# Kernel optimization log

Hardware: AMD Instinct MI355X
Metric: run time of the kernel (lower is better)

The kernel has to match this reference:

```python
import jax, jax.numpy as jnp
import numpy as np
from jax import lax

B, S, HID = 2, 2048, 1024
HK, HV, DK, DV = 16, 16, 64, 64
KCONV = 4
NORM_EPS = 1e-5
KEY_DIM = HK * DK
VAL_DIM = HV * DV
CCH = 2 * KEY_DIM + VAL_DIM  # qkv channels


def setup_inputs() -> dict:
    key = jax.random.key(0)
    ks = jax.random.split(key, 8)
    std = 0.02
    hidden_states = jax.random.normal(ks[0], (B, S, HID), jnp.float32)
    w_qkv = jax.random.normal(ks[1], (CCH, HID), jnp.float32) * std
    w_ab = jax.random.normal(ks[2], (2 * HV + VAL_DIM, HID), jnp.float32) * std
    w_conv = jax.random.normal(ks[3], (CCH, KCONV), jnp.float32) * std  # depthwise kernel
    A_log = jnp.log(jax.random.uniform(ks[4], (HV,), jnp.float32, 1e-3, 16.0))
    dt = jnp.exp(jax.random.uniform(ks[5], (HV,), jnp.float32) * (np.log(0.1) - np.log(0.001)) + np.log(0.001))
    dt = jnp.maximum(dt, 1e-4)
    dt_bias = dt + jnp.log(-jnp.expm1(-dt))
    rms_w = jnp.ones((DV,), jnp.float32)
    w_o = jax.random.normal(ks[6], (HID, VAL_DIM), jnp.float32) * (std / np.sqrt(2 * 24))
    return dict(hidden_states=hidden_states, w_qkv=w_qkv, w_ab=w_ab, w_conv=w_conv,
                A_log=A_log, dt_bias=dt_bias, rms_w=rms_w, w_o=w_o)


def _l2norm(x, eps=1e-6):
    return x * lax.rsqrt(jnp.sum(x * x, axis=-1, keepdims=True) + eps)


def reference(hidden_states, w_qkv, w_ab, w_conv, A_log, dt_bias, rms_w, w_o):
    qkv = hidden_states @ w_qkv.T                       # [B,S,CCH]
    ab = hidden_states @ w_ab.T                         # [B,S,2H+VAL_DIM]
    a = ab[..., :HV]
    b = ab[..., HV:2 * HV]
    gate = ab[..., 2 * HV:]
    # causal depthwise conv1d (kernel KCONV, left pad KCONV-1) + silu
    xp = jnp.pad(qkv, ((0, 0), (KCONV - 1, 0), (0, 0)))
    conv = sum(xp[:, i:i + S, :] * w_conv[:, i] for i in range(KCONV))
    qkv = jax.nn.silu(conv)
    q = qkv[..., :KEY_DIM].reshape(B, S, HK, DK)
    k = qkv[..., KEY_DIM:2 * KEY_DIM].reshape(B, S, HK, DK)
    v = qkv[..., 2 * KEY_DIM:].reshape(B, S, HV, DV)
    # HV == HK -> no repeat_interleave needed
    beta = jax.nn.sigmoid(b)                            # [B,S,H]
    g = -jnp.exp(A_log) * jax.nn.softplus(a + dt_bias)  # [B,S,H]
    q = _l2norm(q)
    k = _l2norm(k)
    scale = DK ** -0.5

    def step(h, x):
        qt, kt, vt, gt, bt = x                          # [B,H,D*] / [B,H]
        h = h * jnp.exp(gt)[..., None, None]            # decay: [B,H,DK,DV]
        kv = jnp.einsum('bhk,bhkv->bhv', kt, h)
        delta = bt[..., None] * (vt - kv)               # delta-rule error
        h = h + jnp.einsum('bhk,bhv->bhkv', kt, delta)  # rank-1 update
        ot = jnp.einsum('bhk,bhkv->bhv', qt * scale, h)
        return h, ot

    xs = (jnp.moveaxis(q, 1, 0), jnp.moveaxis(k, 1, 0), jnp.moveaxis(v, 1, 0),
          jnp.moveaxis(g, 1, 0), jnp.moveaxis(beta, 1, 0))
    h0 = jnp.zeros((B, HV, DK, DV), jnp.float32)
    _, o = lax.scan(step, h0, xs)                       # [S,B,H,DV]
    o = jnp.moveaxis(o, 0, 1)                           # [B,S,H,DV]
    o = o * jax.nn.silu(gate.reshape(B, S, HV, DV))
    o = o * lax.rsqrt(jnp.mean(o * o, axis=-1, keepdims=True) + NORM_EPS) * rms_w
    o = o.reshape(B, S, VAL_DIM) @ w_o.T                # [B,S,HID]
    return o
```

## Files before the change

### kernel.cpp

```cpp
#include <hip/hip_runtime.h>
#include <stdint.h>
#include <math.h>

#define NPAD 4224

typedef float  f32x4_t __attribute__((ext_vector_type(4)));
typedef __bf16 bfx8_t  __attribute__((ext_vector_type(8)));
typedef __bf16 bfx4_t  __attribute__((ext_vector_type(4)));

#define F4(p)  (*reinterpret_cast<const float4*>(p))
#define F4W(p) (*reinterpret_cast<float4*>(p))

__device__ __forceinline__ void gload_lds16(const void* g, void* l) {
  __builtin_amdgcn_global_load_lds((const __attribute__((address_space(1))) void*)g,
                                   (__attribute__((address_space(3))) void*)l, 16, 0, 0);
}

__device__ __forceinline__ float sigmoidf_fast(float x) { return 1.f / (1.f + __expf(-x)); }
__device__ __forceinline__ float siluf(float x) { return x * sigmoidf_fast(x); }

__device__ __forceinline__ float allreduce64(float v) {
#pragma unroll
  for (int m = 1; m < 64; m <<= 1) v += __shfl_xor(v, m, 64);
  return v;
}

__device__ __forceinline__ bfx4_t to_bf4(float4 v) {
  bfx4_t o; o[0] = (__bf16)v.x; o[1] = (__bf16)v.y; o[2] = (__bf16)v.z; o[3] = (__bf16)v.w;
  return o;
}

__device__ __forceinline__ uint32_t bf2pack(float a, float b) {
  union { __bf16 h[2]; uint32_t u; } x;
  x.h[0] = (__bf16)a; x.h[1] = (__bf16)b; return x.u;
}

__global__ __launch_bounds__(256) void cvt_f32_bf16(const float* __restrict__ in,
                                                    __bf16* __restrict__ out) {
  int i = blockIdx.x * 256 + threadIdx.x;
  float4 v = reinterpret_cast<const float4*>(in)[i];
  reinterpret_cast<bfx4_t*>(out)[i] = to_bf4(v);
}

__global__ __launch_bounds__(256) void cvt_weights(const float* __restrict__ wqkv,
                                                   const float* __restrict__ wab,
                                                   __bf16* __restrict__ Wb) {
  int i = blockIdx.x * 256 + threadIdx.x;
  int e = i * 4;
  int row = e >> 10, col = e & 1023;
  float4 v;
  if (row < 3072)      v = *reinterpret_cast<const float4*>(wqkv + e);
  else if (row < 4128) v = *reinterpret_cast<const float4*>(wab + ((row - 3072) << 10) + col);
  else                 v = make_float4(0.f, 0.f, 0.f, 0.f);
  reinterpret_cast<bfx4_t*>(Wb)[i] = to_bf4(v);
}

__global__ __launch_bounds__(256, 2) void gemm_bt(const __bf16* __restrict__ A,
                                                  const __bf16* __restrict__ Bm,
                                                  float* __restrict__ C,
                                                  int K, int lda, int ldb, int ldc) {
  __shared__ __align__(16) __bf16 As[128 * 64];
  __shared__ __align__(16) __bf16 Bs[128 * 64];
  const int tid = threadIdx.x;
  const int w = tid >> 6, lane = tid & 63;
  const int tm = blockIdx.x & 31, tn = blockIdx.x >> 5;
  const int wr = w >> 1, wc = w & 1;
  const int srow = lane >> 3, scol = (lane & 7) * 8;

  f32x4_t acc[4][4];
#pragma unroll
  for (int i = 0; i < 4; i++)
#pragma unroll
    for (int j = 0; j < 4; j++) acc[i][j] = f32x4_t{0.f, 0.f, 0.f, 0.f};

  const __bf16* Abase = A + (size_t)(tm * 128 + srow) * lda + scol;
  const __bf16* Bbase = Bm + (size_t)(tn * 128 + srow) * ldb + scol;

  for (int kk = 0; kk < K; kk += 64) {
#pragma unroll
    for (int r = 0; r < 4; r++) {
      const int rr = (r * 4 + w) * 8;
      gload_lds16(Abase + (size_t)rr * lda + kk, &As[rr * 64]);
      gload_lds16(Bbase + (size_t)rr * ldb + kk, &Bs[rr * 64]);
    }
    __syncthreads();
#pragma unroll
    for (int ks = 0; ks < 2; ks++) {
      bfx8_t af[4], bfr[4];
#pragma unroll
      for (int i = 0; i < 4; i++) {
        af[i]  = *reinterpret_cast<const bfx8_t*>(&As[(wr * 64 + i * 16 + (lane & 15)) * 64 + ks * 32 + (lane >> 4) * 8]);
        bfr[i] = *reinterpret_cast<const bfx8_t*>(&Bs[(wc * 64 + i * 16 + (lane & 15)) * 64 + ks * 32 + (lane >> 4) * 8]);
      }
#pragma unroll
      for (int i = 0; i < 4; i++)
#pragma unroll
        for (int j = 0; j < 4; j++)
          acc[i][j] = __builtin_amdgcn_mfma_f32_16x16x32_bf16(af[i], bfr[j], acc[i][j], 0, 0, 0);
    }
    __syncthreads();
  }
  const int crow = tm * 128 + wr * 64 + (lane >> 4) * 4;
  const int ccol = tn * 128 + wc * 64 + (lane & 15);
#pragma unroll
  for (int i = 0; i < 4; i++)
#pragma unroll
    for (int j = 0; j < 4; j++)
#pragma unroll
      for (int r = 0; r < 4; r++)
        C[(size_t)(crow + i * 16 + r) * ldc + ccol + j * 16] = acc[i][j][r];
}

__global__ __launch_bounds__(256, 2) void gemm_bt_b16(const __bf16* __restrict__ A,
                                                      const __bf16* __restrict__ Bm,
                                                      __bf16* __restrict__ C,
                                                      int K, int lda, int ldb, int ldc) {
  __shared__ __align__(16) __bf16 As[128 * 64];
  __shared__ __align__(16) __bf16 Bs[128 * 64];
  const int tid = threadIdx.x;
  const int w = tid >> 6, lane = tid & 63;
  const int tm = blockIdx.x & 31, tn = blockIdx.x >> 5;
  const int wr = w >> 1, wc = w & 1;
  const int srow = lane >> 3, scol = (lane & 7) * 8;

  f32x4_t acc[4][4];
#pragma unroll
  for (int i = 0; i < 4; i++)
#pragma unroll
    for (int j = 0; j < 4; j++) acc[i][j] = f32x4_t{0.f, 0.f, 0.f, 0.f};

  const __bf16* Abase = A + (size_t)(tm * 128 + srow) * lda + scol;
  const __bf16* Bbase = Bm + (size_t)(tn * 128 + srow) * ldb + scol;

  for (int kk = 0; kk < K; kk += 64) {
#pragma unroll
    for (int r = 0; r < 4; r++) {
      const int rr = (r * 4 + w) * 8;
      gload_lds16(Abase + (size_t)rr * lda + kk, &As[rr * 64]);
      gload_lds16(Bbase + (size_t)rr * ldb + kk, &Bs[rr * 64]);
    }
    __syncthreads();
#pragma unroll
    for (int ks = 0; ks < 2; ks++) {
      bfx8_t af[4], bfr[4];
#pragma unroll
      for (int i = 0; i < 4; i++) {
        af[i]  = *reinterpret_cast<const bfx8_t*>(&As[(wr * 64 + i * 16 + (lane & 15)) * 64 + ks * 32 + (lane >> 4) * 8]);
        bfr[i] = *reinterpret_cast<const bfx8_t*>(&Bs[(wc * 64 + i * 16 + (lane & 15)) * 64 + ks * 32 + (lane >> 4) * 8]);
      }
#pragma unroll
      for (int i = 0; i < 4; i++)
#pragma unroll
        for (int j = 0; j < 4; j++)
          acc[i][j] = __builtin_amdgcn_mfma_f32_16x16x32_bf16(af[i], bfr[j], acc[i][j], 0, 0, 0);
    }
    __syncthreads();
  }
  const int crow = tm * 128 + wr * 64 + (lane >> 4) * 4;
  const int ccol = tn * 128 + wc * 64 + (lane & 15);
#pragma unroll
  for (int i = 0; i < 4; i++)
#pragma unroll
    for (int j = 0; j < 4; j++)
#pragma unroll
      for (int r = 0; r < 4; r++)
        C[(size_t)(crow + i * 16 + r) * ldc + ccol + j * 16] = (__bf16)acc[i][j][r];
}

__global__ __launch_bounds__(256) void prep_kernel(
    const __bf16* __restrict__ Y, const float* __restrict__ w_conv,
    const float* __restrict__ A_log, const float* __restrict__ dt_bias,
    float* __restrict__ qs, float* __restrict__ ks_, float* __restrict__ vs,
    float* __restrict__ gbuf, float* __restrict__ bbuf) {
  const int blk = blockIdx.x;
  const int b = blk >> 11, s = blk & 2047;
  const int tid = threadIdx.x;
  const int w = tid >> 6, lane = tid & 63;

  float x[12];
#pragma unroll
  for (int j = 0; j < 12; j++) {
    const int c = tid + 256 * j;
    const float4 wc = *reinterpret_cast<const float4*>(w_conv + c * 4);
    const float* wcp = reinterpret_cast<const float*>(&wc);
    float acc = 0.f;
#pragma unroll
    for (int i = 0; i < 4; i++) {
      const int r = s - 3 + i;
      const float v = (r >= 0) ? (float)Y[(size_t)(b * 2048 + r) * NPAD + c] : 0.f;
      acc = fmaf(v, wcp[i], acc);
    }
    x[j] = siluf(acc);
  }

#pragma unroll
  for (int j = 0; j < 4; j++) {
    const float sq = allreduce64(x[j] * x[j]);
    const float sk = allreduce64(x[j + 4] * x[j + 4]);
    const float rq = rsqrtf(sq + 1e-6f) * 0.125f;
    const float rk = rsqrtf(sk + 1e-6f);
    const int head = 4 * j + w;
    const size_t base = ((size_t)(b * 16 + head) * 2048 + s) * 64 + lane;
    qs[base] = x[j] * rq;
    ks_[base] = x[j + 4] * rk;
    vs[base] = x[8 + j];
  }

  const __bf16* yab = Y + (size_t)blk * NPAD + 3072;
  if (tid < 16) {
    float a = (float)yab[tid] + dt_bias[tid];
    float sp = (a > 20.f) ? a : log1pf(expf(a));
    gbuf[(size_t)(b * 16 + tid) * 2048 + s] = -expf(A_log[tid]) * sp;
  } else if (tid < 32) {
    int t = tid - 16;
    bbuf[(size_t)(b * 16 + t) * 2048 + s] = 1.f / (1.f + expf(-(float)yab[16 + t]));
  }
}


__global__ __launch_bounds__(256, 3) void chunkA(
    const float* __restrict__ ks_, const float* __restrict__ vs,
    const float* __restrict__ gbuf, const float* __restrict__ bbuf,
    float* __restrict__ Dvg, __bf16* __restrict__ Wgb,
    float* __restrict__ Mg, float* __restrict__ PTg, float* __restrict__ egb) {
  const int task = blockIdx.x, bh = task >> 5, cc = task & 31;
  const int tid = threadIdx.x;
  const int w = tid >> 6, lane = tid & 63;
  __shared__ __align__(16) char regA[18432];
  __shared__ __align__(16) float Ks[64 * 68];
  __shared__ __align__(16) char regC[9216];
  __shared__ float xbc[2][128];
  __shared__ float gcs[64], bcs[64];
  float* At   = (float*)regA;
  __bf16* XTb = (__bf16*)regA;
  __bf16* Kb   = (__bf16*)regC;
  __bf16* KdTb = (__bf16*)regC;

  const size_t cb = ((size_t)bh * 2048 + cc * 64) * 64;
  { int s = tid >> 2, d0 = (tid & 3) * 16;
#pragma unroll
    for (int i = 0; i < 4; i++) {
      float4 v = F4(&ks_[cb + (size_t)s * 64 + d0 + 4 * i]);
      F4W(&Ks[s * 68 + d0 + 4 * i]) = v;
      *reinterpret_cast<bfx4_t*>(&Kb[s * 72 + d0 + 4 * i]) = to_bf4(v);
    }
  }
  if (tid < 64) {
    float gv = gbuf[(size_t)bh * 2048 + cc * 64 + tid];
    bcs[tid] = bbuf[(size_t)bh * 2048 + cc * 64 + tid];
#pragma unroll
    for (int off = 1; off < 64; off <<= 1) {
      float n = __shfl_up(gv, (unsigned)off, 64);
      if (tid >= off) gv += n;
    }
    gcs[tid] = gv;
  }
  __syncthreads();

  const int hh = tid >> 7, cI = tid & 127;
  float vpre[32];
  if (cI < 64) {
#pragma unroll
    for (int r = 0; r < 32; r++)
      vpre[r] = vs[cb + (size_t)(hh * 32 + r) * 64 + cI];
  }

  {
    bfx8_t aS[2];
#pragma unroll
    for (int kh = 0; kh < 2; kh++)
      aS[kh] = *reinterpret_cast<const bfx8_t*>(&Kb[(16 * w + (lane & 15)) * 72 + kh * 32 + (lane >> 4) * 8]);
#pragma unroll
    for (int j = 0; j < 4; j++) {
      if (j < w) {
#pragma unroll
        for (int r = 0; r < 4; r++)
          At[(16 * w + (lane >> 4) * 4 + r) * 68 + 16 * j + (lane & 15)] = 0.f;
      } else {
        f32x4_t acc = {0.f, 0.f, 0.f, 0.f};
#pragma unroll
        for (int kh = 0; kh < 2; kh++) {
          bfx8_t bS = *reinterpret_cast<const bfx8_t*>(&Kb[(16 * j + (lane & 15)) * 72 + kh * 32 + (lane >> 4) * 8]);
          acc = __builtin_amdgcn_mfma_f32_16x16x32_bf16(aS[kh], bS, acc, 0, 0, 0);
        }
        const int t = 16 * j + (lane & 15);
        const float bt = bcs[t], gt = gcs[t];
#pragma unroll
        for (int r = 0; r < 4; r++) {
          const int s = 16 * w + (lane >> 4) * 4 + r;
          At[s * 68 + t] = (t > s) ? bt * __expf(gt - gcs[s]) * acc[r] : 0.f;
        }
      }
    }
  }
  __syncthreads();

  float X[32];
  if (cI < 64) {
#pragma unroll
    for (int r = 0; r < 32; r++) X[r] = bcs[hh * 32 + r] * vpre[r];
  } else {
#pragma unroll
    for (int r = 0; r < 32; r++) {
      int s = hh * 32 + r;
      X[r] = bcs[s] * __expf(gcs[s]) * Ks[s * 68 + (cI - 64)];
    }
  }

#pragma unroll
  for (int s = 0; s < 64; ++s) {
    if (hh == (s >> 5)) xbc[s & 1][cI] = X[s & 31];
    __syncthreads();
    float xs = xbc[s & 1][cI];
    const float* atrow = &At[s * 68 + hh * 32];
#pragma unroll
    for (int j = 0; j < 8; j++) {
      float4 a4 = F4(atrow + 4 * j);
      X[4 * j + 0] = fmaf(-a4.x, xs, X[4 * j + 0]);
      X[4 * j + 1] = fmaf(-a4.y, xs, X[4 * j + 1]);
      X[4 * j + 2] = fmaf(-a4.z, xs, X[4 * j + 2]);
      X[4 * j + 3] = fmaf(-a4.w, xs, X[4 * j + 3]);
    }
  }
  __syncthreads();

  if (cI < 64) {
#pragma unroll
    for (int r = 0; r < 32; r++)
      Dvg[(size_t)task * 4096 + (size_t)(hh * 32 + r) * 64 + cI] = X[r];
  } else {
#pragma unroll
    for (int r = 0; r < 32; r++)
      Wgb[(size_t)task * 4096 + (size_t)(hh * 32 + r) * 64 + (cI - 64)] = (__bf16)X[r];
  }
#pragma unroll
  for (int i = 0; i < 16; i++)
    *reinterpret_cast<uint32_t*>(&XTb[cI * 72 + hh * 32 + 2 * i]) = bf2pack(X[2 * i], X[2 * i + 1]);
  {
    int s = tid >> 2, d0 = (tid & 3) * 16;
    float ek = __expf(gcs[63] - gcs[s]);
#pragma unroll
    for (int i = 0; i < 4; i++) {
      float4 v = F4(&Ks[s * 68 + d0 + 4 * i]);
      KdTb[(d0 + 4 * i + 0) * 72 + s] = (__bf16)(v.x * ek);
      KdTb[(d0 + 4 * i + 1) * 72 + s] = (__bf16)(v.y * ek);
      KdTb[(d0 + 4 * i + 2) * 72 + s] = (__bf16)(v.z * ek);
      KdTb[(d0 + 4 * i + 3) * 72 + s] = (__bf16)(v.w * ek);
    }
  }
  __syncthreads();

  {
    bfx8_t aM[2], aP[2];
#pragma unroll
    for (int kh = 0; kh < 2; kh++) {
      aM[kh] = *reinterpret_cast<const bfx8_t*>(&KdTb[(16 * w + (lane & 15)) * 72 + kh * 32 + (lane >> 4) * 8]);
      aP[kh] = *reinterpret_cast<const bfx8_t*>(&XTb [(16 * w + (lane & 15)) * 72 + kh * 32 + (lane >> 4) * 8]);
    }
#pragma unroll
    for (int j = 0; j < 4; j++) {
      f32x4_t mAcc = {0.f, 0.f, 0.f, 0.f}, pAcc = {0.f, 0.f, 0.f, 0.f};
#pragma unroll
      for (int kh = 0; kh < 2; kh++) {
        bfx8_t bW = *reinterpret_cast<const bfx8_t*>(&XTb [(64 + 16 * j + (lane & 15)) * 72 + kh * 32 + (lane >> 4) * 8]);
        bfx8_t bK = *reinterpret_cast<const bfx8_t*>(&KdTb[(16 * j + (lane & 15)) * 72 + kh * 32 + (lane >> 4) * 8]);
        mAcc = __builtin_amdgcn_mfma_f32_16x16x32_bf16(aM[kh], bW, mAcc, 0, 0, 0);
        pAcc = __builtin_amdgcn_mfma_f32_16x16x32_bf16(aP[kh], bK, pAcc, 0, 0, 0);
      }
#pragma unroll
      for (int r = 0; r < 4; r++) {
        const int drow = 16 * w + (lane >> 4) * 4 + r;
        const int ecol = 16 * j + (lane & 15);
        const int ge = ecol >> 2;
        const int ges = (ge & 8) | ((ge & 7) ^ (drow & 7));
        Mg [(size_t)task * 4096 + drow * 64 + ges * 4 + (ecol & 3)] = mAcc[r];
        PTg[(size_t)task * 4096 + drow * 64 + ecol] = pAcc[r];
      }
    }
  }
  if (tid == 0) egb[task] = __expf(gcs[63]);
}

__global__ __launch_bounds__(64) void chunkB(
    const float* __restrict__ Mg, const float* __restrict__ PTg,
    const float* __restrict__ egb, float* __restrict__ hTg) {
  const int bh = blockIdx.x & 31, vq = blockIdx.x >> 5;
  const int tid = threadIdx.x;
  const int tv = tid >> 4, td = tid & 15;
  __shared__ __align__(16) float Ml[2][64 * 64];
  __shared__ __align__(16) float hT[8 * 68];

  float h[2][4];
#pragma unroll
  for (int r = 0; r < 2; r++)
#pragma unroll
    for (int c = 0; c < 4; c++) h[r][c] = 0.f;
#pragma unroll
  for (int r = 0; r < 2; r++)
#pragma unroll
    for (int c = 0; c < 4; c++) hT[(tv * 2 + r) * 68 + c * 16 + td] = 0.f;

  const char* mb = (const char*)(Mg + (size_t)bh * 32 * 4096);
#pragma unroll
  for (int j = 0; j < 16; j++)
    gload_lds16(mb + j * 1024 + tid * 16, &Ml[0][j * 256]);

  const int kk = (td & 7) << 2;
  int cur = 0;
  for (int cch = 0; cch < 32; ++cch) {
    const size_t tb = ((size_t)bh * 32 + cch) * 4096;
    asm volatile("s_waitcnt vmcnt(0)" ::: "memory");
    __builtin_amdgcn_sched_barrier(0);
    if (cch < 31) {
#pragma unroll
      for (int j = 0; j < 16; j++)
        gload_lds16(mb + (size_t)(cch + 1) * 16384 + j * 1024 + tid * 16,
                    &Ml[cur ^ 1][j * 256]);
    }
    float ptc[2][4];
#pragma unroll
    for (int r = 0; r < 2; r++)
#pragma unroll
      for (int c = 0; c < 4; c++)
        ptc[r][c] = PTg[tb + (size_t)(vq * 8 + tv * 2 + r) * 64 + c * 16 + td];
    const float egc = egb[bh * 32 + cch];
#pragma unroll
    for (int r = 0; r < 2; r++)
#pragma unroll
      for (int c = 0; c < 4; c++)
        hTg[tb + (size_t)(vq * 8 + tv * 2 + r) * 64 + c * 16 + td] = h[r][c];
    float acc[2][4] = {};
#pragma unroll
    for (int e0 = 0; e0 < 64; e0 += 4) {
      const int es = (e0 & 32) | ((e0 & 28) ^ kk);
      float4 h4[2], m4[4];
#pragma unroll
      for (int r = 0; r < 2; r++) h4[r] = F4(&hT[(tv * 2 + r) * 68 + e0]);
#pragma unroll
      for (int c = 0; c < 4; c++) m4[c] = F4(&Ml[cur][(c * 16 + td) * 64 + es]);
#pragma unroll
      for (int r = 0; r < 2; r++)
#pragma unroll
        for (int c = 0; c < 4; c++) {
          acc[r][c] = fmaf(h4[r].x, m4[c].x, acc[r][c]);
          acc[r][c] = fmaf(h4[r].y, m4[c].y, acc[r][c]);
          acc[r][c] = fmaf(h4[r].z, m4[c].z, acc[r][c]);
          acc[r][c] = fmaf(h4[r].w, m4[c].w, acc[r][c]);
        }
    }
#pragma unroll
    for (int r = 0; r < 2; r++)
#pragma unroll
      for (int c = 0; c < 4; c++)
        h[r][c] = egc * h[r][c] - acc[r][c] + ptc[r][c];
#pragma unroll
    for (int r = 0; r < 2; r++)
#pragma unroll
      for (int c = 0; c < 4; c++) hT[(tv * 2 + r) * 68 + c * 16 + td] = h[r][c];
    cur ^= 1;
  }
}

__global__ __launch_bounds__(256, 3) void chunkC(
    const float* __restrict__ qs, const float* __restrict__ ks_,
    const float* __restrict__ gbuf, const float* __restrict__ Dvg,
    const __bf16* __restrict__ Wgb, const float* __restrict__ hTg,
    float* __restrict__ o_raw) {
  const int task = blockIdx.x, bh = task >> 5, cc = task & 31;
  const int b = bh >> 4, hd = bh & 15;
  const int tid = threadIdx.x;
  const int w = tid >> 6, lane = tid & 63;
  __shared__ __align__(16) __bf16 cQb[64 * 72];
  __shared__ __align__(16) char  regK[9216];
  __shared__ __align__(16) __bf16 cWb[64 * 72];
  __shared__ __align__(16) __bf16 hTb[64 * 72];
  __shared__ __align__(16) __bf16 Smb[64 * 72];
  __shared__ float gcs[64];
  __bf16* cKb = (__bf16*)regK;
  __bf16* dTb = (__bf16*)regK;

  const size_t cb = ((size_t)bh * 2048 + cc * 64) * 64;
  { int s = tid >> 2, d0 = (tid & 3) * 16;
#pragma unroll
    for (int i = 0; i < 4; i++) {
      *reinterpret_cast<bfx4_t*>(&cQb[s * 72 + d0 + 4 * i]) = to_bf4(F4(&qs [cb + (size_t)s * 64 + d0 + 4 * i]));
      *reinterpret_cast<bfx4_t*>(&cKb[s * 72 + d0 + 4 * i]) = to_bf4(F4(&ks_[cb + (size_t)s * 64 + d0 + 4 * i]));
      *reinterpret_cast<bfx4_t*>(&hTb[s * 72 + d0 + 4 * i]) = to_bf4(F4(&hTg[(size_t)task * 4096 + (size_t)s * 64 + d0 + 4 * i]));
    }
    const bfx8_t* wp = reinterpret_cast<const bfx8_t*>(&Wgb[(size_t)task * 4096 + (size_t)s * 64 + d0]);
    *reinterpret_cast<bfx8_t*>(&cWb[s * 72 + d0]) = wp[0];
    *reinterpret_cast<bfx8_t*>(&cWb[s * 72 + d0 + 8]) = wp[1];
  }
  if (tid < 64) {
    float gv = gbuf[(size_t)bh * 2048 + cc * 64 + tid];
#pragma unroll
    for (int off = 1; off < 64; off <<= 1) {
      float n = __shfl_up(gv, (unsigned)off, 64);
      if (tid >= off) gv += n;
    }
    gcs[tid] = gv;
  }
  __syncthreads();

  f32x4_t qh[4];
  {
    bfx8_t aQ[2];
#pragma unroll
    for (int kh = 0; kh < 2; kh++)
      aQ[kh] = *reinterpret_cast<const bfx8_t*>(&cQb[(16 * w + (lane & 15)) * 72 + kh * 32 + (lane >> 4) * 8]);
#pragma unroll
    for (int j = 0; j < 4; j++) {
      f32x4_t sAcc = {0.f, 0.f, 0.f, 0.f};
      qh[j] = f32x4_t{0.f, 0.f, 0.f, 0.f};
#pragma unroll
      for (int kh = 0; kh < 2; kh++) {
        bfx8_t bK = *reinterpret_cast<const bfx8_t*>(&cKb[(16 * j + (lane & 15)) * 72 + kh * 32 + (lane >> 4) * 8]);
        bfx8_t bH = *reinterpret_cast<const bfx8_t*>(&hTb[(16 * j + (lane & 15)) * 72 + kh * 32 + (lane >> 4) * 8]);
        sAcc = __builtin_amdgcn_mfma_f32_16x16x32_bf16(aQ[kh], bK, sAcc, 0, 0, 0);
        qh[j] = __builtin_amdgcn_mfma_f32_16x16x32_bf16(aQ[kh], bH, qh[j], 0, 0, 0);
      }
      const int s = 16 * j + (lane & 15);
      const float gs = gcs[s];
#pragma unroll
      for (int r = 0; r < 4; r++) {
        const int t = 16 * w + (lane >> 4) * 4 + r;
        float sv = (s <= t) ? __expf(gcs[t] - gs) * sAcc[r] : 0.f;
        Smb[t * 72 + s] = (__bf16)sv;
      }
    }
  }
  __syncthreads();

  {
    bfx8_t aW[2];
#pragma unroll
    for (int kh = 0; kh < 2; kh++)
      aW[kh] = *reinterpret_cast<const bfx8_t*>(&cWb[(16 * w + (lane & 15)) * 72 + kh * 32 + (lane >> 4) * 8]);
#pragma unroll
    for (int j = 0; j < 4; j++) {
      f32x4_t u = {0.f, 0.f, 0.f, 0.f};
#pragma unroll
      for (int kh = 0; kh < 2; kh++) {
        bfx8_t bH = *reinterpret_cast<const bfx8_t*>(&hTb[(16 * j + (lane & 15)) * 72 + kh * 32 + (lane >> 4) * 8]);
        u = __builtin_amdgcn_mfma_f32_16x16x32_bf16(aW[kh], bH, u, 0, 0, 0);
      }
      const int v = 16 * j + (lane & 15);
#pragma unroll
      for (int r = 0; r < 4; r++) {
        const int s = 16 * w + (lane >> 4) * 4 + r;
        float dl = Dvg[(size_t)task * 4096 + (size_t)s * 64 + v] - u[r];
        dTb[v * 72 + s] = (__bf16)dl;
      }
    }
  }
  __syncthreads();

  {
    bfx8_t aS2[2];
#pragma unroll
    for (int kh = 0; kh < 2; kh++)
      aS2[kh] = *reinterpret_cast<const bfx8_t*>(&Smb[(16 * w + (lane & 15)) * 72 + kh * 32 + (lane >> 4) * 8]);
    float esc[4];
#pragma unroll
    for (int r = 0; r < 4; r++) esc[r] = __expf(gcs[16 * w + (lane >> 4) * 4 + r]);
#pragma unroll
    for (int j = 0; j < 4; j++) {
#pragma unroll
      for (int r = 0; r < 4; r++) qh[j][r] *= esc[r];
#pragma unroll
      for (int kh = 0; kh < 2; kh++) {
        bfx8_t bD = *reinterpret_cast<const bfx8_t*>(&dTb[(16 * j + (lane & 15)) * 72 + kh * 32 + (lane >> 4) * 8]);
        qh[j] = __builtin_amdgcn_mfma_f32_16x16x32_bf16(aS2[kh], bD, qh[j], 0, 0, 0);
      }
      const int v = 16 * j + (lane & 15);
#pragma unroll
      for (int r = 0; r < 4; r++) {
        const int t = 16 * w + (lane >> 4) * 4 + r;
        o_raw[(((size_t)b * 2048 + cc * 64 + t) * 16 + hd) * 64 + v] = qh[j][r];
      }
    }
  }
}

__global__ __launch_bounds__(256) void gate_rms(
    const float* __restrict__ o_raw, const __bf16* __restrict__ Y,
    const float* __restrict__ rms_w, __bf16* __restrict__ o2b) {
  const int blk = blockIdx.x;
  const int tid = threadIdx.x;
  const int H = tid >> 4, d0 = (tid & 15) * 4;
  const size_t ob = (size_t)blk * 1024 + H * 64 + d0;
  float4 o = *reinterpret_cast<const float4*>(o_raw + ob);
  bfx4_t gb = *reinterpret_cast<const bfx4_t*>(Y + (size_t)blk * NPAD + 3104 + H * 64 + d0);
  float o2[4];
  o2[0] = o.x * siluf((float)gb[0]); o2[1] = o.y * siluf((float)gb[1]);
  o2[2] = o.z * siluf((float)gb[2]); o2[3] = o.w * siluf((float)gb[3]);
  float ssq = o2[0] * o2[0] + o2[1] * o2[1] + o2[2] * o2[2] + o2[3] * o2[3];
  ssq += __shfl_xor(ssq, 1, 64);
  ssq += __shfl_xor(ssq, 2, 64);
  ssq += __shfl_xor(ssq, 4, 64);
  ssq += __shfl_xor(ssq, 8, 64);
  const float scale = rsqrtf(ssq * (1.f / 64.f) + 1e-5f);
  bfx4_t r;
#pragma unroll
  for (int i = 0; i < 4; i++) r[i] = (__bf16)(o2[i] * scale * rms_w[d0 + i]);
  *reinterpret_cast<bfx4_t*>(o2b + ob) = r;
}

extern "C" void kernel_launch(void* const* d_in, const int* in_sizes, int n_in,
                              void* d_out, int out_size, void* d_ws, size_t ws_size,
                              hipStream_t stream) {
  (void)in_sizes; (void)n_in; (void)out_size; (void)ws_size;
  const float* hidden = (const float*)d_in[0];
  const float* w_qkv  = (const float*)d_in[1];
  const float* w_ab   = (const float*)d_in[2];
  const float* w_conv = (const float*)d_in[3];
  const float* A_log  = (const float*)d_in[4];
  const float* dt_b   = (const float*)d_in[5];
  const float* rms_w  = (const float*)d_in[6];
  const float* w_o    = (const float*)d_in[7];
  float* out = (float*)d_out;

  char* ws = (char*)d_ws;
  size_t off = 0;
  auto alloc = [&](size_t bytes) { void* p = ws + off; off += (bytes + 255) & ~(size_t)255; return p; };
  __bf16* Xb   = (__bf16*)alloc((size_t)4096 * 1024 * 2);
  __bf16* Wb   = (__bf16*)alloc((size_t)NPAD * 1024 * 2);
  __bf16* Wob  = (__bf16*)alloc((size_t)1024 * 1024 * 2);
  __bf16* Y    = (__bf16*)alloc((size_t)4096 * NPAD * 2);
  float* qs    = (float*)alloc((size_t)32 * 2048 * 64 * 4);
  float* ks    = (float*)alloc((size_t)32 * 2048 * 64 * 4);
  float* vs    = (float*)alloc((size_t)32 * 2048 * 64 * 4);
  float* gbuf  = (float*)alloc((size_t)32 * 2048 * 4);
  float* bbuf  = (float*)alloc((size_t)32 * 2048 * 4);
  float* Dvg   = (float*)alloc((size_t)1024 * 4096 * 4);
  __bf16* Wgb  = (__bf16*)alloc((size_t)1024 * 4096 * 2);
  float* Mg    = (float*)alloc((size_t)1024 * 4096 * 4);
  float* PTg   = (float*)alloc((size_t)1024 * 4096 * 4);
  float* hTg   = (float*)alloc((size_t)1024 * 4096 * 4);
  float* egb   = (float*)alloc((size_t)1024 * 4);
  __bf16* o2b  = (__bf16*)alloc((size_t)4096 * 1024 * 2);
  float* o_raw = (float*)Xb;

  cvt_f32_bf16<<<4096, 256, 0, stream>>>(hidden, Xb);
  cvt_weights<<<4224, 256, 0, stream>>>(w_qkv, w_ab, Wb);
  cvt_f32_bf16<<<1024, 256, 0, stream>>>(w_o, Wob);
  gemm_bt_b16<<<32 * 33, 256, 0, stream>>>(Xb, Wb, Y, 1024, 1024, 1024, NPAD);
  prep_kernel<<<4096, 256, 0, stream>>>(Y, w_conv, A_log, dt_b, qs, ks, vs, gbuf, bbuf);
  chunkA<<<1024, 256, 0, stream>>>(ks, vs, gbuf, bbuf, Dvg, Wgb, Mg, PTg, egb);
  chunkB<<<256, 64, 0, stream>>>(Mg, PTg, egb, hTg);
  chunkC<<<1024, 256, 0, stream>>>(qs, ks, gbuf, Dvg, Wgb, hTg, o_raw);
  gate_rms<<<4096, 256, 0, stream>>>(o_raw, Y, rms_w, o2b);
  gemm_bt<<<32 * 8, 256, 0, stream>>>(o2b, Wob, out, 1024, 1024, 1024, 1024);
}
```

Baseline: 359.8 us.

## Store q/k/v intermediates in bf16 and vectorize prep kernel

The prep kernel now writes q, k and v as bf16 instead of fp32. Each thread handles 8 contiguous channels with 16-byte loads and does the per-head L2 norm through 8-lane shuffles rather than full 64-lane allreduces. chunkA and chunkC read bf16 directly, which removes the fp32 K shared-memory copy and one barrier, and chunkA's occupancy hint rises from 3 to 4 blocks. This halves the bytes written and read for q/k/v but rounds v and k to bf16 earlier, slightly changing numerics in the fp32 paths that previously used fp32 k/v.

```diff
diff --git a/kernel.cpp b/kernel.cpp
--- a/kernel.cpp
+++ b/kernel.cpp
@@ -10,6 +10,8 @@
 
 #define F4(p)  (*reinterpret_cast<const float4*>(p))
 #define F4W(p) (*reinterpret_cast<float4*>(p))
+#define BF8(p)  (*reinterpret_cast<const bfx8_t*>(p))
+#define BF8W(p) (*reinterpret_cast<bfx8_t*>(p))
 
 __device__ __forceinline__ void gload_lds16(const void* g, void* l) {
   __builtin_amdgcn_global_load_lds((const __attribute__((address_space(1))) void*)g,
@@ -18,12 +20,6 @@
 
 __device__ __forceinline__ float sigmoidf_fast(float x) { return 1.f / (1.f + __expf(-x)); }
 __device__ __forceinline__ float siluf(float x) { return x * sigmoidf_fast(x); }
-
-__device__ __forceinline__ float allreduce64(float v) {
-#pragma unroll
-  for (int m = 1; m < 64; m <<= 1) v += __shfl_xor(v, m, 64);
-  return v;
-}
 
 __device__ __forceinline__ bfx4_t to_bf4(float4 v) {
   bfx4_t o; o[0] = (__bf16)v.x; o[1] = (__bf16)v.y; o[2] = (__bf16)v.z; o[3] = (__bf16)v.w;
@@ -89,8 +85,8 @@
       bfx8_t af[4], bfr[4];
 #pragma unroll
       for (int i = 0; i < 4; i++) {
-        af[i]  = *reinterpret_cast<const bfx8_t*>(&As[(wr * 64 + i * 16 + (lane & 15)) * 64 + ks * 32 + (lane >> 4) * 8]);
-        bfr[i] = *reinterpret_cast<const bfx8_t*>(&Bs[(wc * 64 + i * 16 + (lane & 15)) * 64 + ks * 32 + (lane >> 4) * 8]);
+        af[i]  = BF8(&As[(wr * 64 + i * 16 + (lane & 15)) * 64 + ks * 32 + (lane >> 4) * 8]);
+        bfr[i] = BF8(&Bs[(wc * 64 + i * 16 + (lane & 15)) * 64 + ks * 32 + (lane >> 4) * 8]);
       }
 #pragma unroll
       for (int i = 0; i < 4; i++)
@@ -145,8 +141,8 @@
       bfx8_t af[4], bfr[4];
 #pragma unroll
       for (int i = 0; i < 4; i++) {
-        af[i]  = *reinterpret_cast<const bfx8_t*>(&As[(wr * 64 + i * 16 + (lane & 15)) * 64 + ks * 32 + (lane >> 4) * 8]);
-        bfr[i] = *reinterpret_cast<const bfx8_t*>(&Bs[(wc * 64 + i * 16 + (lane & 15)) * 64 + ks * 32 + (lane >> 4) * 8]);
+        af[i]  = BF8(&As[(wr * 64 + i * 16 + (lane & 15)) * 64 + ks * 32 + (lane >> 4) * 8]);
+        bfr[i] = BF8(&Bs[(wc * 64 + i * 16 + (lane & 15)) * 64 + ks * 32 + (lane >> 4) * 8]);
       }
 #pragma unroll
       for (int i = 0; i < 4; i++)
@@ -167,43 +163,56 @@
         C[(size_t)(crow + i * 16 + r) * ldc + ccol + j * 16] = (__bf16)acc[i][j][r];
 }
 
-__global__ __launch_bounds__(256) void prep_kernel(
+__global__ __launch_bounds__(384) void prep_kernel(
     const __bf16* __restrict__ Y, const float* __restrict__ w_conv,
     const float* __restrict__ A_log, const float* __restrict__ dt_bias,
-    float* __restrict__ qs, float* __restrict__ ks_, float* __restrict__ vs,
+    __bf16* __restrict__ qs, __bf16* __restrict__ ks_, __bf16* __restrict__ vs,
     float* __restrict__ gbuf, float* __restrict__ bbuf) {
   const int blk = blockIdx.x;
   const int b = blk >> 11, s = blk & 2047;
   const int tid = threadIdx.x;
-  const int w = tid >> 6, lane = tid & 63;
-
-  float x[12];
-#pragma unroll
-  for (int j = 0; j < 12; j++) {
-    const int c = tid + 256 * j;
-    const float4 wc = *reinterpret_cast<const float4*>(w_conv + c * 4);
-    const float* wcp = reinterpret_cast<const float*>(&wc);
-    float acc = 0.f;
-#pragma unroll
-    for (int i = 0; i < 4; i++) {
-      const int r = s - 3 + i;
-      const float v = (r >= 0) ? (float)Y[(size_t)(b * 2048 + r) * NPAD + c] : 0.f;
-      acc = fmaf(v, wcp[i], acc);
-    }
-    x[j] = siluf(acc);
-  }
-
-#pragma unroll
-  for (int j = 0; j < 4; j++) {
-    const float sq = allreduce64(x[j] * x[j]);
-    const float sk = allreduce64(x[j + 4] * x[j + 4]);
-    const float rq = rsqrtf(sq + 1e-6f) * 0.125f;
-    const float rk = rsqrtf(sk + 1e-6f);
-    const int head = 4 * j + w;
-    const size_t base = ((size_t)(b * 16 + head) * 2048 + s) * 64 + lane;
-    qs[base] = x[j] * rq;
-    ks_[base] = x[j + 4] * rk;
-    vs[base] = x[8 + j];
+  const int c0 = tid * 8;
+
+  bfx8_t yv[4], z8;
+#pragma unroll
+  for (int q = 0; q < 8; q++) z8[q] = (__bf16)0.f;
+#pragma unroll
+  for (int i = 0; i < 4; i++) {
+    const int r = s - 3 + i;
+    yv[i] = (r >= 0) ? BF8(&Y[(size_t)(b * 2048 + r) * NPAD + c0]) : z8;
+  }
+  float x[8];
+#pragma unroll
+  for (int q = 0; q < 8; q++) {
+    const float4 wq = F4(&w_conv[(c0 + q) * 4]);
+    float acc = fmaf((float)yv[0][q], wq.x,
+                fmaf((float)yv[1][q], wq.y,
+                fmaf((float)yv[2][q], wq.z, (float)yv[3][q] * wq.w)));
+    x[q] = siluf(acc);
+  }
+
+  const int sec = tid >> 7;
+  const int head = (tid >> 3) & 15;
+  const int d0 = (tid & 7) * 8;
+  const size_t base = ((size_t)(b * 16 + head) * 2048 + s) * 64 + d0;
+  bfx8_t outv;
+  if (sec < 2) {
+    float ss = 0.f;
+#pragma unroll
+    for (int q = 0; q < 8; q++) ss = fmaf(x[q], x[q], ss);
+    ss += __shfl_xor(ss, 1, 64);
+    ss += __shfl_xor(ss, 2, 64);
+    ss += __shfl_xor(ss, 4, 64);
+    float rs = rsqrtf(ss + 1e-6f);
+    if (sec == 0) rs *= 0.125f;
+#pragma unroll
+    for (int q = 0; q < 8; q++) outv[q] = (__bf16)(x[q] * rs);
+    if (sec == 0) BF8W(&qs[base]) = outv;
+    else          BF8W(&ks_[base]) = outv;
+  } else {
+#pragma unroll
+    for (int q = 0; q < 8; q++) outv[q] = (__bf16)x[q];
+    BF8W(&vs[base]) = outv;
   }
 
   const __bf16* yab = Y + (size_t)blk * NPAD + 3072;
@@ -218,8 +227,8 @@
 }
 
 
-__global__ __launch_bounds__(256, 3) void chunkA(
-    const float* __restrict__ ks_, const float* __restrict__ vs,
+__global__ __launch_bounds__(256, 4) void chunkA(
+    const __bf16* __restrict__ ks_, const __bf16* __restrict__ vs,
     const float* __restrict__ gbuf, const float* __restrict__ bbuf,
     float* __restrict__ Dvg, __bf16* __restrict__ Wgb,
     float* __restrict__ Mg, float* __restrict__ PTg, float* __restrict__ egb) {
@@ -227,7 +236,6 @@
   const int tid = threadIdx.x;
   const int w = tid >> 6, lane = tid & 63;
   __shared__ __align__(16) char regA[18432];
-  __shared__ __align__(16) float Ks[64 * 68];
   __shared__ __align__(16) char regC[9216];
   __shared__ float xbc[2][128];
   __shared__ float gcs[64], bcs[64];
@@ -237,14 +245,11 @@
   __bf16* KdTb = (__bf16*)regC;
 
   const size_t cb = ((size_t)bh * 2048 + cc * 64) * 64;
-  { int s = tid >> 2, d0 = (tid & 3) * 16;
-#pragma unroll
-    for (int i = 0; i < 4; i++) {
-      float4 v = F4(&ks_[cb + (size_t)s * 64 + d0 + 4 * i]);
-      F4W(&Ks[s * 68 + d0 + 4 * i]) = v;
-      *reinterpret_cast<bfx4_t*>(&Kb[s * 72 + d0 + 4 * i]) = to_bf4(v);
-    }
-  }
+  const int sr = tid >> 2, sd0 = (tid & 3) * 16;
+  bfx8_t kst0 = BF8(&ks_[cb + (size_t)sr * 64 + sd0]);
+  bfx8_t kst1 = BF8(&ks_[cb + (size_t)sr * 64 + sd0 + 8]);
+  BF8W(&Kb[sr * 72 + sd0]) = kst0;
+  BF8W(&Kb[sr * 72 + sd0 + 8]) = kst1;
   if (tid < 64) {
     float gv = gbuf[(size_t)bh * 2048 + cc * 64 + tid];
     bcs[tid] = bbuf[(size_t)bh * 2048 + cc * 64 + tid];
@@ -262,14 +267,14 @@
   if (cI < 64) {
 #pragma unroll
     for (int r = 0; r < 32; r++)
-      vpre[r] = vs[cb + (size_t)(hh * 32 + r) * 64 + cI];
+      vpre[r] = (float)vs[cb + (size_t)(hh * 32 + r) * 64 + cI];
   }
 
   {
     bfx8_t aS[2];
 #pragma unroll
     for (int kh = 0; kh < 2; kh++)
-      aS[kh] = *reinterpret_cast<const bfx8_t*>(&Kb[(16 * w + (lane & 15)) * 72 + kh * 32 + (lane >> 4) * 8]);
+      aS[kh] = BF8(&Kb[(16 * w + (lane & 15)) * 72 + kh * 32 + (lane >> 4) * 8]);
 #pragma unroll
     for (int j = 0; j < 4; j++) {
       if (j < w) {
@@ -280,7 +285,7 @@
         f32x4_t acc = {0.f, 0.f, 0.f, 0.f};
 #pragma unroll
         for (int kh = 0; kh < 2; kh++) {
-          bfx8_t bS = *reinterpret_cast<const bfx8_t*>(&Kb[(16 * j + (lane & 15)) * 72 + kh * 32 + (lane >> 4) * 8]);
+          bfx8_t bS = BF8(&Kb[(16 * j + (lane & 15)) * 72 + kh * 32 + (lane >> 4) * 8]);
           acc = __builtin_amdgcn_mfma_f32_16x16x32_bf16(aS[kh], bS, acc, 0, 0, 0);
         }
         const int t = 16 * j + (lane & 15);
@@ -293,7 +298,6 @@
       }
     }
   }
-  __syncthreads();
 
   float X[32];
   if (cI < 64) {
@@ -303,7 +307,7 @@
 #pragma unroll
     for (int r = 0; r < 32; r++) {
       int s = hh * 32 + r;
-      X[r] = bcs[s] * __expf(gcs[s]) * Ks[s * 68 + (cI - 64)];
+      X[r] = bcs[s] * __expf(gcs[s]) * (float)Kb[s * 72 + (cI - 64)];
     }
   }
 
@@ -337,15 +341,11 @@
   for (int i = 0; i < 16; i++)
     *reinterpret_cast<uint32_t*>(&XTb[cI * 72 + hh * 32 + 2 * i]) = bf2pack(X[2 * i], X[2 * i + 1]);
   {
-    int s = tid >> 2, d0 = (tid & 3) * 16;
-    float ek = __expf(gcs[63] - gcs[s]);
-#pragma unroll
-    for (int i = 0; i < 4; i++) {
-      float4 v = F4(&Ks[s * 68 + d0 + 4 * i]);
-      KdTb[(d0 + 4 * i + 0) * 72 + s] = (__bf16)(v.x * ek);
-      KdTb[(d0 + 4 * i + 1) * 72 + s] = (__bf16)(v.y * ek);
-      KdTb[(d0 + 4 * i + 2) * 72 + s] = (__bf16)(v.z * ek);
-      KdTb[(d0 + 4 * i + 3) * 72 + s] = (__bf16)(v.w * ek);
+    const float ek = __expf(gcs[63] - gcs[sr]);
+#pragma unroll
+    for (int i = 0; i < 8; i++) {
+      KdTb[(sd0 + i) * 72 + sr]     = (__bf16)((float)kst0[i] * ek);
+      KdTb[(sd0 + 8 + i) * 72 + sr] = (__bf16)((float)kst1[i] * ek);
     }
   }
   __syncthreads();
@@ -354,16 +354,16 @@
     bfx8_t aM[2], aP[2];
 #pragma unroll
     for (int kh = 0; kh < 2; kh++) {
-      aM[kh] = *reinterpret_cast<const bfx8_t*>(&KdTb[(16 * w + (lane & 15)) * 72 + kh * 32 + (lane >> 4) * 8]);
-      aP[kh] = *reinterpret_cast<const bfx8_t*>(&XTb [(16 * w + (lane & 15)) * 72 + kh * 32 + (lane >> 4) * 8]);
+      aM[kh] = BF8(&KdTb[(16 * w + (lane & 15)) * 72 + kh * 32 + (lane >> 4) * 8]);
+      aP[kh] = BF8(&XTb [(16 * w + (lane & 15)) * 72 + kh * 32 + (lane >> 4) * 8]);
     }
 #pragma unroll
     for (int j = 0; j < 4; j++) {
       f32x4_t mAcc = {0.f, 0.f, 0.f, 0.f}, pAcc = {0.f, 0.f, 0.f, 0.f};
 #pragma unroll
       for (int kh = 0; kh < 2; kh++) {
-        bfx8_t bW = *reinterpret_cast<const bfx8_t*>(&XTb [(64 + 16 * j + (lane & 15)) * 72 + kh * 32 + (lane >> 4) * 8]);
-        bfx8_t bK = *reinterpret_cast<const bfx8_t*>(&KdTb[(16 * j + (lane & 15)) * 72 + kh * 32 + (lane >> 4) * 8]);
+        bfx8_t bW = BF8(&XTb [(64 + 16 * j + (lane & 15)) * 72 + kh * 32 + (lane >> 4) * 8]);
+        bfx8_t bK = BF8(&KdTb[(16 * j + (lane & 15)) * 72 + kh * 32 + (lane >> 4) * 8]);
         mAcc = __builtin_amdgcn_mfma_f32_16x16x32_bf16(aM[kh], bW, mAcc, 0, 0, 0);
         pAcc = __builtin_amdgcn_mfma_f32_16x16x32_bf16(aP[kh], bK, pAcc, 0, 0, 0);
       }
@@ -462,7 +462,7 @@
 }
 
 __global__ __launch_bounds__(256, 3) void chunkC(
-    const float* __restrict__ qs, const float* __restrict__ ks_,
+    const __bf16* __restrict__ qs, const __bf16* __restrict__ ks_,
     const float* __restrict__ gbuf, const float* __restrict__ Dvg,
     const __bf16* __restrict__ Wgb, const float* __restrict__ hTg,
     float* __restrict__ o_raw) {
@@ -481,15 +481,16 @@
 
   const size_t cb = ((size_t)bh * 2048 + cc * 64) * 64;
   { int s = tid >> 2, d0 = (tid & 3) * 16;
-#pragma unroll
-    for (int i = 0; i < 4; i++) {
-      *reinterpret_cast<bfx4_t*>(&cQb[s * 72 + d0 + 4 * i]) = to_bf4(F4(&qs [cb + (size_t)s * 64 + d0 + 4 * i]));
-      *reinterpret_cast<bfx4_t*>(&cKb[s * 72 + d0 + 4 * i]) = to_bf4(F4(&ks_[cb + (size_t)s * 64 + d0 + 4 * i]));
-      *reinterpret_cast<bfx4_t*>(&hTb[s * 72 + d0 + 4 * i]) = to_bf4(F4(&hTg[(size_t)task * 4096 + (size_t)s * 64 + d0 + 4 * i]));
-    }
-    const bfx8_t* wp = reinterpret_cast<const bfx8_t*>(&Wgb[(size_t)task * 4096 + (size_t)s * 64 + d0]);
-    *reinterpret_cast<bfx8_t*>(&cWb[s * 72 + d0]) = wp[0];
-    *reinterpret_cast<bfx8_t*>(&cWb[s * 72 + d0 + 8]) = wp[1];
+    BF8W(&cQb[s * 72 + d0])     = BF8(&qs [cb + (size_t)s * 64 + d0]);
+    BF8W(&cQb[s * 72 + d0 + 8]) = BF8(&qs [cb + (size_t)s * 64 + d0 + 8]);
+    BF8W(&cKb[s * 72 + d0])     = BF8(&ks_[cb + (size_t)s * 64 + d0]);
+    BF8W(&cKb[s * 72 + d0 + 8]) = BF8(&ks_[cb + (size_t)s * 64 + d0 + 8]);
+#pragma unroll
+    for (int i = 0; i < 4; i++)
+      *reinterpret_cast<bfx4_t*>(&hTb[s * 72 + d0 + 4 * i]) =
+          to_bf4(F4(&hTg[(size_t)task * 4096 + (size_t)s * 64 + d0 + 4 * i]));
+    BF8W(&cWb[s * 72 + d0])     = BF8(&Wgb[(size_t)task * 4096 + (size_t)s * 64 + d0]);
+    BF8W(&cWb[s * 72 + d0 + 8]) = BF8(&Wgb[(size_t)task * 4096 + (size_t)s * 64 + d0 + 8]);
   }
   if (tid < 64) {
     float gv = gbuf[(size_t)bh * 2048 + cc * 64 + tid];
@@ -507,15 +508,15 @@
     bfx8_t aQ[2];
 #pragma unroll
     for (int kh = 0; kh < 2; kh++)
-      aQ[kh] = *reinterpret_cast<const bfx8_t*>(&cQb[(16 * w + (lane & 15)) * 72 + kh * 32 + (lane >> 4) * 8]);
+      aQ[kh] = BF8(&cQb[(16 * w + (lane & 15)) * 72 + kh * 32 + (lane >> 4) * 8]);
 #pragma unroll
     for (int j = 0; j < 4; j++) {
       f32x4_t sAcc = {0.f, 0.f, 0.f, 0.f};
       qh[j] = f32x4_t{0.f, 0.f, 0.f, 0.f};
 #pragma unroll
       for (int kh = 0; kh < 2; kh++) {
-        bfx8_t bK = *reinterpret_cast<const bfx8_t*>(&cKb[(16 * j + (lane & 15)) * 72 + kh * 32 + (lane >> 4) * 8]);
-        bfx8_t bH = *reinterpret_cast<const bfx8_t*>(&hTb[(16 * j + (lane & 15)) * 72 + kh * 32 + (lane >> 4) * 8]);
+        bfx8_t bK = BF8(&cKb[(16 * j + (lane & 15)) * 72 + kh * 32 + (lane >> 4) * 8]);
+        bfx8_t bH = BF8(&hTb[(16 * j + (lane & 15)) * 72 + kh * 32 + (lane >> 4) * 8]);
         sAcc = __builtin_amdgcn_mfma_f32_16x16x32_bf16(aQ[kh], bK, sAcc, 0, 0, 0);
         qh[j] = __builtin_amdgcn_mfma_f32_16x16x32_bf16(aQ[kh], bH, qh[j], 0, 0, 0);
       }
@@ -535,13 +536,13 @@
     bfx8_t aW[2];
 #pragma unroll
     for (int kh = 0; kh < 2; kh++)
-      aW[kh] = *reinterpret_cast<const bfx8_t*>(&cWb[(16 * w + (lane & 15)) * 72 + kh * 32 + (lane >> 4) * 8]);
+      aW[kh] = BF8(&cWb[(16 * w + (lane & 15)) * 72 + kh * 32 + (lane >> 4) * 8]);
 #pragma unroll
     for (int j = 0; j < 4; j++) {
       f32x4_t u = {0.f, 0.f, 0.f, 0.f};
 #pragma unroll
       for (int kh = 0; kh < 2; kh++) {
-        bfx8_t bH = *reinterpret_cast<const bfx8_t*>(&hTb[(16 * j + (lane & 15)) * 72 + kh * 32 + (lane >> 4) * 8]);
+        bfx8_t bH = BF8(&hTb[(16 * j + (lane & 15)) * 72 + kh * 32 + (lane >> 4) * 8]);
         u = __builtin_amdgcn_mfma_f32_16x16x32_bf16(aW[kh], bH, u, 0, 0, 0);
       }
       const int v = 16 * j + (lane & 15);
@@ -559,7 +560,7 @@
     bfx8_t aS2[2];
 #pragma unroll
     for (int kh = 0; kh < 2; kh++)
-      aS2[kh] = *reinterpret_cast<const bfx8_t*>(&Smb[(16 * w + (lane & 15)) * 72 + kh * 32 + (lane >> 4) * 8]);
+      aS2[kh] = BF8(&Smb[(16 * w + (lane & 15)) * 72 + kh * 32 + (lane >> 4) * 8]);
     float esc[4];
 #pragma unroll
     for (int r = 0; r < 4; r++) esc[r] = __expf(gcs[16 * w + (lane >> 4) * 4 + r]);
@@ -569,7 +570,7 @@
       for (int r = 0; r < 4; r++) qh[j][r] *= esc[r];
 #pragma unroll
       for (int kh = 0; kh < 2; kh++) {
-        bfx8_t bD = *reinterpret_cast<const bfx8_t*>(&dTb[(16 * j + (lane & 15)) * 72 + kh * 32 + (lane >> 4) * 8]);
+        bfx8_t bD = BF8(&dTb[(16 * j + (lane & 15)) * 72 + kh * 32 + (lane >> 4) * 8]);
         qh[j] = __builtin_amdgcn_mfma_f32_16x16x32_bf16(aS2[kh], bD, qh[j], 0, 0, 0);
       }
       const int v = 16 * j + (lane & 15);
@@ -627,9 +628,9 @@
   __bf16* Wb   = (__bf16*)alloc((size_t)NPAD * 1024 * 2);
   __bf16* Wob  = (__bf16*)alloc((size_t)1024 * 1024 * 2);
   __bf16* Y    = (__bf16*)alloc((size_t)4096 * NPAD * 2);
-  float* qs    = (float*)alloc((size_t)32 * 2048 * 64 * 4);
-  float* ks    = (float*)alloc((size_t)32 * 2048 * 64 * 4);
-  float* vs    = (float*)alloc((size_t)32 * 2048 * 64 * 4);
+  __bf16* qs   = (__bf16*)alloc((size_t)32 * 2048 * 64 * 2);
+  __bf16* ks   = (__bf16*)alloc((size_t)32 * 2048 * 64 * 2);
+  __bf16* vs   = (__bf16*)alloc((size_t)32 * 2048 * 64 * 2);
   float* gbuf  = (float*)alloc((size_t)32 * 2048 * 4);
   float* bbuf  = (float*)alloc((size_t)32 * 2048 * 4);
   float* Dvg   = (float*)alloc((size_t)1024 * 4096 * 4);
@@ -645,7 +646,7 @@
   cvt_weights<<<4224, 256, 0, stream>>>(w_qkv, w_ab, Wb);
   cvt_f32_bf16<<<1024, 256, 0, stream>>>(w_o, Wob);
   gemm_bt_b16<<<32 * 33, 256, 0, stream>>>(Xb, Wb, Y, 1024, 1024, 1024, NPAD);
-  prep_kernel<<<4096, 256, 0, stream>>>(Y, w_conv, A_log, dt_b, qs, ks, vs, gbuf, bbuf);
+  prep_kernel<<<4096, 384, 0, stream>>>(Y, w_conv, A_log, dt_b, qs, ks, vs, gbuf, bbuf);
   chunkA<<<1024, 256, 0, stream>>>(ks, vs, gbuf, bbuf, Dvg, Wgb, Mg, PTg, egb);
   chunkB<<<256, 64, 0, stream>>>(Mg, PTg, egb, hTg);
   chunkC<<<1024, 256, 0, stream>>>(qs, ks, gbuf, Dvg, Wgb, hTg, o_raw);
```

New measurement: 324.4 us. -9.8%, faster.
